# Performance work log

Hardware: AMD Instinct MI355X
Metric: run time of the kernel (lower is better)

The kernel has to match this reference:

```python
import jax, jax.numpy as jnp
import numpy as np

NUM_TREES = 100
VOCAB = 100000
DIM = 32            # dim_leaf_emb
ATT = DIM // 2      # att_dim = 16
BS = 1024

# pair indices matching itertools.combinations(range(n), 2)
_ROW, _COL = np.triu_indices(NUM_TREES, k=1)


def setup_inputs() -> dict:
    key = jax.random.key(0)
    ks = jax.random.split(key, 12)
    x = jax.random.randint(ks[0], (BS, NUM_TREES), 0, VOCAB)
    Emb = jax.random.normal(ks[1], (VOCAB, DIM), dtype=jnp.float32) * 0.02
    W = jax.random.normal(ks[2], (DIM, ATT), dtype=jnp.float32) * (1.0 / np.sqrt(DIM))
    b = jnp.zeros((ATT,), dtype=jnp.float32)
    h = jax.random.normal(ks[3], (ATT,), dtype=jnp.float32) * 0.1
    W1 = jax.random.normal(ks[4], (DIM, DIM // 2), dtype=jnp.float32) * (1.0 / np.sqrt(DIM))
    b1 = jnp.zeros((DIM // 2,), dtype=jnp.float32)
    W2 = jax.random.normal(ks[5], (DIM // 2, DIM // 4), dtype=jnp.float32) * (1.0 / np.sqrt(DIM // 2))
    b2 = jnp.zeros((DIM // 4,), dtype=jnp.float32)
    Wf = jax.random.normal(ks[6], (DIM // 4, 1), dtype=jnp.float32) * (1.0 / np.sqrt(DIM // 4))
    bf = jnp.zeros((1,), dtype=jnp.float32)
    return {"x": x, "Emb": Emb, "W": W, "b": b, "h": h,
            "W1": W1, "b1": b1, "W2": W2, "b2": b2, "Wf": Wf, "bf": bf}


def reference(x, Emb, W, b, h, W1, b1, W2, b2, Wf, bf):
    e = Emb[x]                                   # (bs, T, D)
    half_bip = e[:, _ROW] * e[:, _COL]           # (bs, P, D), P = T*(T-1)/2
    s = jax.nn.relu(jnp.einsum('bpd,da->bpa', half_bip, W) + b)  # (bs, P, A)
    att = jax.nn.softmax(jnp.einsum('bpa,a->bp', s, h), axis=-1) # (bs, P)
    pooled = jnp.einsum('bpd,bp->bd', half_bip, att)             # (bs, D)
    o = jax.nn.relu(pooled @ W1 + b1)
    o = jax.nn.relu(o @ W2 + b2)
    return jax.nn.sigmoid(o @ Wf + bf)           # (bs, 1)
```

## Files before the change

kernel.cpp:

```cpp
#include <hip/hip_runtime.h>
#include <math.h>

constexpr int kT = 100;
constexpr int kD = 32;
constexpr int kA = 16;
constexpr int kESH = 40;
constexpr int kRows = 116;
constexpr int kNT = 512;

typedef float    float4v __attribute__((ext_vector_type(4)));
typedef __fp16   fp16x2  __attribute__((ext_vector_type(2)));
typedef __fp16   half4   __attribute__((ext_vector_type(4)));
typedef __fp16   half8   __attribute__((ext_vector_type(8)));
typedef _Float16 half4v  __attribute__((ext_vector_type(4)));
typedef _Float16 half8v  __attribute__((ext_vector_type(8)));

#if __has_builtin(__builtin_amdgcn_exp2f)
#define EXP2F(x) __builtin_amdgcn_exp2f(x)
#else
#define EXP2F(x) exp2f(x)
#endif

__global__ __launch_bounds__(kNT, 8)
void afm_kernel(const int* __restrict__ x,
                const float* __restrict__ Emb,
                const float* __restrict__ W,
                const float* __restrict__ bb,
                const float* __restrict__ h,
                const float* __restrict__ W1,
                const float* __restrict__ b1,
                const float* __restrict__ W2,
                const float* __restrict__ b2,
                const float* __restrict__ Wf,
                const float* __restrict__ bf,
                float* __restrict__ out)
{
    __shared__ __align__(16) unsigned char smem[18432];
    __shared__ float sh_pooled[kD];
    __shared__ float sh_o1[kA];
    __shared__ float sh_o2[8];

    __fp16* she = (__fp16*)smem;
    const char* sheb = (const char*)smem;

    const int tid  = threadIdx.x;
    const int b    = blockIdx.x;
    const int lane = tid & 63;
    const int wv   = tid >> 6;
    const int quad = lane >> 4;
    const int l15  = lane & 15;
    const int k0   = quad * 8;

    const int* xb = x + b * kT;
    for (int i = tid; i < kT * 8; i += kNT) {
        const int row = i >> 3, c4 = i & 7;
        const int v = xb[row];
        const float4 val = ((const float4*)Emb)[v * 8 + c4];
        union { fp16x2 h2[2]; half4 h4; } tmp;
        tmp.h2[0] = __builtin_amdgcn_cvt_pkrtz(val.x, val.y);
        tmp.h2[1] = __builtin_amdgcn_cvt_pkrtz(val.z, val.w);
        *(half4*)(she + row * kESH + c4 * 4) = tmp.h4;
    }
    if (tid < (kRows - kT) * kESH / 2)
        ((unsigned int*)she)[kT * kESH / 2 + tid] = 0u;

    union { fp16x2 h2[4]; half8v h8; } wa;
#pragma unroll
    for (int j = 0; j < 4; ++j)
        wa.h2[j] = __builtin_amdgcn_cvt_pkrtz(W[(k0 + 2 * j) * kA + l15],
                                              W[(k0 + 2 * j + 1) * kA + l15]);
    float4v bfrag;
#pragma unroll
    for (int rg = 0; rg < 4; ++rg) bfrag[rg] = bb[quad * 4 + rg];

    union { fp16x2 h2[2]; half4v v; } hf;
    hf.h2[0] = __builtin_amdgcn_cvt_pkrtz(h[quad * 4 + 0] * 1.44269504f,
                                          h[quad * 4 + 1] * 1.44269504f);
    hf.h2[1] = __builtin_amdgcn_cvt_pkrtz(h[quad * 4 + 2] * 1.44269504f,
                                          h[quad * 4 + 3] * 1.44269504f);
    const float4v zero4 = {0.0f, 0.0f, 0.0f, 0.0f};

    const int lane_base = l15 * 80 + quad * 16;
    __syncthreads();

    fp16x2 pool2[4];
    const fp16x2 zz = {(__fp16)0.0f, (__fp16)0.0f};
#pragma unroll
    for (int j = 0; j < 4; ++j) pool2[j] = zz;
    float lsum = 0.0f;

    union HB { half8 fp; fp16x2 h2[4]; half8v mf; };

    auto do_tile = [&](const half8& er, int coff, int rem, bool mask) {
        HB hb;
        hb.fp = er * (*(const half8*)(sheb + coff));
        float4v s1 = __builtin_amdgcn_mfma_f32_16x16x32_f16(wa.h8, hb.mf, bfrag, 0, 0, 0);
        union { fp16x2 h2[2]; half4v v; } rl;
        rl.h2[0] = __builtin_amdgcn_cvt_pkrtz(fmaxf(s1[0], 0.0f), fmaxf(s1[1], 0.0f));
        rl.h2[1] = __builtin_amdgcn_cvt_pkrtz(fmaxf(s1[2], 0.0f), fmaxf(s1[3], 0.0f));
        float4v l4 = __builtin_amdgcn_mfma_f32_16x16x16f16(hf.v, rl.v, zero4, 0, 0, 0);
        float w = EXP2F(l4[0]);
        if (mask) w = (l15 < rem) ? w : 0.0f;
        lsum += w;
        const fp16x2 ww = __builtin_amdgcn_cvt_pkrtz(w, w);
#pragma unroll
        for (int j = 0; j < 4; ++j)
            pool2[j] += ww * hb.h2[j];
    };

    auto do_row = [&](int r) {
        const int len = 99 - r;
        const int nfull = (len - 1) >> 4;
        const half8 er = *(const half8*)(sheb + r * 80 + quad * 16);
        int coff = (r + 1) * 80 + lane_base;
        for (int j = 0; j < nfull; ++j, coff += 1280)
            do_tile(er, coff, 16, false);
        do_tile(er, coff, len - (nfull << 4), true);
    };

    for (int g = 0; g < 6; ++g) {
        const int wvg = (wv + g) & 7;
        do_row(g * 16 + wvg);
        do_row(g * 16 + 15 - wvg);
    }
    if (wv < 3) do_row(96 + wv);

    __syncthreads();
    float* stg = (float*)smem;
#pragma unroll
    for (int j = 0; j < 4; ++j) {
        stg[tid * 9 + 2 * j]     = (float)pool2[j][0];
        stg[tid * 9 + 2 * j + 1] = (float)pool2[j][1];
    }
    stg[tid * 9 + 8] = lsum;
    __syncthreads();

    if (tid < kD) {
        const int q = tid >> 3, j = tid & 7;
        float s = 0.0f, sw = 0.0f;
        for (int w8 = 0; w8 < 8; ++w8)
            for (int l = 0; l < 16; ++l) {
                const float* row = stg + (w8 * 64 + q * 16 + l) * 9;
                s += row[j];
                sw += row[8];
            }
        sh_pooled[tid] = s / sw;
    }
    __syncthreads();

    if (tid < kA) {
        float o = b1[tid];
#pragma unroll
        for (int d = 0; d < kD; ++d) o = fmaf(sh_pooled[d], W1[d * kA + tid], o);
        sh_o1[tid] = fmaxf(o, 0.0f);
    }
    __syncthreads();
    if (tid < 8) {
        float o = b2[tid];
#pragma unroll
        for (int a = 0; a < kA; ++a) o = fmaf(sh_o1[a], W2[a * 8 + tid], o);
        sh_o2[tid] = fmaxf(o, 0.0f);
    }
    __syncthreads();
    if (tid == 0) {
        float z = bf[0];
#pragma unroll
        for (int j = 0; j < 8; ++j) z = fmaf(sh_o2[j], Wf[j], z);
        out[b] = 1.0f / (1.0f + __expf(-z));
    }
}

extern "C" void kernel_launch(void* const* d_in, const int* in_sizes, int n_in,
                              void* d_out, int out_size, void* d_ws, size_t ws_size,
                              hipStream_t stream) {
    const int*   x   = (const int*)d_in[0];
    const float* Emb = (const float*)d_in[1];
    const float* W   = (const float*)d_in[2];
    const float* bb  = (const float*)d_in[3];
    const float* h   = (const float*)d_in[4];
    const float* W1  = (const float*)d_in[5];
    const float* b1  = (const float*)d_in[6];
    const float* W2  = (const float*)d_in[7];
    const float* b2  = (const float*)d_in[8];
    const float* Wf  = (const float*)d_in[9];
    const float* bf  = (const float*)d_in[10];
    float* out = (float*)d_out;

    afm_kernel<<<1024, kNT, 0, stream>>>(x, Emb, W, bb, h, W1, b1, W2, b2, Wf, bf, out);
}
```

Before: 104.7 us.

## Factor row embedding out of pair products and prefetch next column tile

Result: slower. 242.8 us (+131.8%).

```diff
diff --git a/kernel.cpp b/kernel.cpp
--- a/kernel.cpp
+++ b/kernel.cpp
@@ -5,7 +5,7 @@
 constexpr int kD = 32;
 constexpr int kA = 16;
 constexpr int kESH = 40;
-constexpr int kRows = 116;
+constexpr int kRows = 132;
 constexpr int kNT = 512;
 
 typedef float    float4v __attribute__((ext_vector_type(4)));
@@ -61,10 +61,10 @@
         tmp.h2[1] = __builtin_amdgcn_cvt_pkrtz(val.z, val.w);
         *(half4*)(she + row * kESH + c4 * 4) = tmp.h4;
     }
-    if (tid < (kRows - kT) * kESH / 2)
+    if (tid < 16 * kESH / 2)
         ((unsigned int*)she)[kT * kESH / 2 + tid] = 0u;
 
-    union { fp16x2 h2[4]; half8v h8; } wa;
+    union { fp16x2 h2[4]; half8 fp; half8v h8; } wa;
 #pragma unroll
     for (int j = 0; j < 4; ++j)
         wa.h2[j] = __builtin_amdgcn_cvt_pkrtz(W[(k0 + 2 * j) * kA + l15],
@@ -89,33 +89,37 @@
     for (int j = 0; j < 4; ++j) pool2[j] = zz;
     float lsum = 0.0f;
 
-    union HB { half8 fp; fp16x2 h2[4]; half8v mf; };
-
-    auto do_tile = [&](const half8& er, int coff, int rem, bool mask) {
-        HB hb;
-        hb.fp = er * (*(const half8*)(sheb + coff));
-        float4v s1 = __builtin_amdgcn_mfma_f32_16x16x32_f16(wa.h8, hb.mf, bfrag, 0, 0, 0);
-        union { fp16x2 h2[2]; half4v v; } rl;
-        rl.h2[0] = __builtin_amdgcn_cvt_pkrtz(fmaxf(s1[0], 0.0f), fmaxf(s1[1], 0.0f));
-        rl.h2[1] = __builtin_amdgcn_cvt_pkrtz(fmaxf(s1[2], 0.0f), fmaxf(s1[3], 0.0f));
-        float4v l4 = __builtin_amdgcn_mfma_f32_16x16x16f16(hf.v, rl.v, zero4, 0, 0, 0);
-        float w = EXP2F(l4[0]);
-        if (mask) w = (l15 < rem) ? w : 0.0f;
-        lsum += w;
-        const fp16x2 ww = __builtin_amdgcn_cvt_pkrtz(w, w);
-#pragma unroll
-        for (int j = 0; j < 4; ++j)
-            pool2[j] += ww * hb.h2[j];
-    };
+    union E8 { half8 fp; fp16x2 h2[4]; half8v mf; };
 
     auto do_row = [&](int r) {
         const int len = 99 - r;
-        const int nfull = (len - 1) >> 4;
-        const half8 er = *(const half8*)(sheb + r * 80 + quad * 16);
+        const int ntiles = (len + 15) >> 4;
+        const int rem = len - ((ntiles - 1) << 4);
+        E8 er; er.fp = *(const half8*)(sheb + r * 80 + quad * 16);
+        E8 ap; ap.fp = wa.fp * er.fp;
         int coff = (r + 1) * 80 + lane_base;
-        for (int j = 0; j < nfull; ++j, coff += 1280)
-            do_tile(er, coff, 16, false);
-        do_tile(er, coff, len - (nfull << 4), true);
+        E8 ec; ec.fp = *(const half8*)(sheb + coff);
+        fp16x2 accu[4];
+#pragma unroll
+        for (int j = 0; j < 4; ++j) accu[j] = zz;
+        for (int t = 0; t < ntiles; ++t) {
+            const half8 ecn = *(const half8*)(sheb + coff + 1280);
+            coff += 1280;
+            float4v s1 = __builtin_amdgcn_mfma_f32_16x16x32_f16(ap.mf, ec.mf, bfrag, 0, 0, 0);
+            union { fp16x2 h2[2]; half4v v; } rl;
+            rl.h2[0] = __builtin_amdgcn_cvt_pkrtz(fmaxf(s1[0], 0.0f), fmaxf(s1[1], 0.0f));
+            rl.h2[1] = __builtin_amdgcn_cvt_pkrtz(fmaxf(s1[2], 0.0f), fmaxf(s1[3], 0.0f));
+            float4v l4 = __builtin_amdgcn_mfma_f32_16x16x16f16(hf.v, rl.v, zero4, 0, 0, 0);
+            float w = EXP2F(l4[0]);
+            if (t == ntiles - 1) w = (l15 < rem) ? w : 0.0f;
+            lsum += w;
+            const fp16x2 ww = __builtin_amdgcn_cvt_pkrtz(w, w);
+#pragma unroll
+            for (int j = 0; j < 4; ++j) accu[j] += ww * ec.h2[j];
+            ec.fp = ecn;
+        }
+#pragma unroll
+        for (int j = 0; j < 4; ++j) pool2[j] += er.h2[j] * accu[j];
     };
 
     for (int g = 0; g < 6; ++g) {
```
